# Optimization experiments

Hardware: AMD Instinct MI355X
Metric: run time of the kernel (lower is better)

## Reference

```python
import jax, jax.numpy as jnp
import numpy as np

EMBED_DIM = 1024
NUM_HEADS = 16
HEAD_DIM = EMBED_DIM // NUM_HEADS


def setup_inputs() -> dict:
    key = jax.random.key(0)
    ks = jax.random.split(key, 6)
    s = 1.0 / np.sqrt(EMBED_DIM)
    x = jax.random.normal(ks[0], (2, 2048, EMBED_DIM), dtype=jnp.float32)
    Wk = jax.random.uniform(ks[1], (EMBED_DIM, EMBED_DIM), jnp.float32, -s, s)
    Wq = jax.random.uniform(ks[2], (EMBED_DIM, EMBED_DIM), jnp.float32, -s, s)
    Wv = jax.random.uniform(ks[3], (EMBED_DIM, EMBED_DIM), jnp.float32, -s, s)
    Wo = jax.random.uniform(ks[4], (EMBED_DIM, EMBED_DIM), jnp.float32, -s, s)
    bo = jax.random.uniform(ks[5], (EMBED_DIM,), jnp.float32, -s, s)
    return {"x": x, "Wq": Wq, "Wk": Wk, "Wv": Wv, "Wo": Wo, "bo": bo}


def reference(x, Wq, Wk, Wv, Wo, bo):
    b, s, e = x.shape
    h, d = NUM_HEADS, HEAD_DIM
    scale = d ** (-0.5)
    # nn.Linear: y = x @ W.T ; here W stored as [out, in] -> use W.T
    q = (x @ Wq.T).reshape(b, s, h, d).transpose(0, 2, 1, 3)  # b h s d
    k = (x @ Wk.T).reshape(b, s, h, d).transpose(0, 2, 1, 3)
    v = (x @ Wv.T).reshape(b, s, h, d).transpose(0, 2, 1, 3)
    logits = jnp.einsum('bhqd,bhkd->bhqk', q, k) * scale
    attn = jax.nn.softmax(logits, axis=-1)
    out = jnp.einsum('bhqk,bhkd->bhqd', attn, v)
    out = out.transpose(0, 2, 1, 3).reshape(b, s, e)
    return out @ Wo.T + bo
```

## Files before the change

### kernel.cpp

```cpp
#include <hip/hip_runtime.h>
#include <hip/hip_bf16.h>

using short8 = __attribute__((ext_vector_type(8))) short;
using f32x4  = __attribute__((ext_vector_type(4))) float;
using uint4v = __attribute__((ext_vector_type(4))) unsigned;

#if __has_builtin(__builtin_amdgcn_exp2f)
#define EXP2(x) __builtin_amdgcn_exp2f(x)
#else
#define EXP2(x) exp2f(x)
#endif

#define SOFT_BARRIER()                                            \
    do {                                                          \
        asm volatile("s_waitcnt lgkmcnt(0)" ::: "memory");        \
        __builtin_amdgcn_s_barrier();                             \
    } while (0)

__device__ __forceinline__ short f2bf(float f) {
    union { float f; unsigned u; } v; v.f = f;
    unsigned r = v.u + 0x7fffu + ((v.u >> 16) & 1u);
    return (short)(r >> 16);
}
__device__ __forceinline__ unsigned pack_trunc(float a, float b) {
    union { float f; unsigned u; } ua, ub; ua.f = a; ub.f = b;
#if __has_builtin(__builtin_amdgcn_perm)
    return __builtin_amdgcn_perm(ub.u, ua.u, 0x07060302u);
#else
    return (ub.u & 0xFFFF0000u) | (ua.u >> 16);
#endif
}
__device__ __forceinline__ void async_copy16(const short* g, short* s) {
    __builtin_amdgcn_global_load_lds(
        (const __attribute__((address_space(1))) void*)g,
        (__attribute__((address_space(3))) void*)s, 16, 0, 0);
}

__global__ __launch_bounds__(256) void cvt_f32_bf16(
    const float* __restrict__ s0, const float* __restrict__ s1,
    const float* __restrict__ s2, const float* __restrict__ s3,
    const float* __restrict__ s4,
    short* __restrict__ d0, short* __restrict__ d1, short* __restrict__ d2,
    short* __restrict__ d3, short* __restrict__ d4) {
    const int bid = blockIdx.x;
    const float* s; short* d; int base;
    if (bid < 4096) {
        s = s0; d = d0; base = bid << 10;
    } else {
        const int r = bid - 4096;
        base = (r & 1023) << 10;
        switch (r >> 10) {
            case 0: s = s1; d = d1; break;
            case 1: s = s2; d = d2; break;
            case 2: s = s3; d = d3; break;
            default: s = s4; d = d4; break;
        }
    }
    const int idx = base + threadIdx.x * 4;
    float4 v = *(const float4*)(s + idx);
    short4 o;
    o.x = f2bf(v.x); o.y = f2bf(v.y); o.z = f2bf(v.z); o.w = f2bf(v.w);
    *(short4*)(d + idx) = o;
}

template <int MODE>
__device__ __forceinline__ void gemm_body(const short* __restrict__ A,
                                          const short* __restrict__ B,
                                          short* __restrict__ C,
                                          float scale,
                                          short* __restrict__ As,
                                          short* __restrict__ Bs) {
    constexpr int Kd = 1024, Nd = 1024, Sd = 2048;

    const int tid  = threadIdx.x;
    const int w    = tid >> 6, lane = tid & 63;
    const int quad = lane >> 4, l16 = lane & 15;
    const int xr   = l16 & 7;
    const int wm   = (w >> 1) * 64, wn = (w & 1) * 64;
    const int bm   = blockIdx.y * 128, bn = blockIdx.x * 128;

    f32x4 acc[4][4];
#pragma unroll
    for (int i = 0; i < 4; ++i)
#pragma unroll
        for (int j = 0; j < 4; ++j) acc[i][j] = (f32x4){0.f, 0.f, 0.f, 0.f};

    for (int k0 = 0; k0 < Kd; k0 += 64) {
        __syncthreads();
#pragma unroll
        for (int c = 0; c < 4; ++c) {
            int li   = c * 256 + tid;
            int row  = li >> 3;
            int gcol = ((li & 7) ^ (row & 7)) * 8;
            async_copy16(A + (size_t)(bm + row) * Kd + k0 + gcol, &As[li * 8]);
            async_copy16(B + (size_t)(bn + row) * Kd + k0 + gcol, &Bs[li * 8]);
        }
        __syncthreads();

#pragma unroll
        for (int kk = 0; kk < 2; ++kk) {
            short8 af[4], bfv[4];
#pragma unroll
            for (int mi = 0; mi < 4; ++mi) {
                const int r = wm + mi * 16 + l16;
                af[mi] = *(const short8*)(
                    &As[r * 64 + (((kk * 4 + quad) ^ xr) * 8)]);
            }
#pragma unroll
            for (int ni = 0; ni < 4; ++ni) {
                const int r = wn + ni * 16 + l16;
                bfv[ni] = *(const short8*)(
                    &Bs[r * 64 + (((kk * 4 + quad) ^ xr) * 8)]);
            }
#pragma unroll
            for (int mi = 0; mi < 4; ++mi)
#pragma unroll
                for (int ni = 0; ni < 4; ++ni) {
                    if constexpr (MODE == 2)
                        acc[mi][ni] = __builtin_amdgcn_mfma_f32_16x16x32_bf16(
                            bfv[ni], af[mi], acc[mi][ni], 0, 0, 0);
                    else
                        acc[mi][ni] = __builtin_amdgcn_mfma_f32_16x16x32_bf16(
                            af[mi], bfv[ni], acc[mi][ni], 0, 0, 0);
                }
        }
    }

    if constexpr (MODE == 2) {
#pragma unroll
        for (int mi = 0; mi < 4; ++mi) {
            const int m_g = bm + wm + mi * 16 + l16;
            const int b_  = m_g >> 11, s_ = m_g & 2047;
#pragma unroll
            for (int ni = 0; ni < 4; ++ni)
#pragma unroll
                for (int r = 0; r < 4; ++r) {
                    const int n_g = bn + wn + ni * 16 + quad * 4 + r;
                    C[(size_t)b_ * Nd * Sd + (size_t)n_g * Sd + s_] =
                        f2bf(acc[mi][ni][r]);
                }
        }
    } else {
#pragma unroll
        for (int ni = 0; ni < 4; ++ni) {
            const int colg = bn + wn + ni * 16 + l16;
#pragma unroll
            for (int mi = 0; mi < 4; ++mi)
#pragma unroll
                for (int r = 0; r < 4; ++r) {
                    const int rowg = bm + wm + mi * 16 + quad * 4 + r;
                    C[(size_t)rowg * Nd + colg] = f2bf(acc[mi][ni][r] * scale);
                }
        }
    }
}

#define CSC 0.18033688f

__global__ __launch_bounds__(256, 3) void proj_gemm(
    const short* __restrict__ X,
    const short* __restrict__ Wq, const short* __restrict__ Wk,
    const short* __restrict__ Wv,
    short* __restrict__ Qo, short* __restrict__ Ko, short* __restrict__ VTo) {
    __shared__ __align__(16) short As[128 * 64];
    __shared__ __align__(16) short Bs[128 * 64];
    if (blockIdx.z == 0)
        gemm_body<0>(X, Wq, Qo, CSC, As, Bs);
    else if (blockIdx.z == 1)
        gemm_body<0>(X, Wk, Ko, 1.0f, As, Bs);
    else
        gemm_body<2>(X, Wv, VTo, 1.0f, As, Bs);
}

__global__ __launch_bounds__(256, 2) void out_gemm(
    const short* __restrict__ A, const short* __restrict__ B,
    const float* __restrict__ bias, float* __restrict__ C) {
    constexpr int Kd = 1024, Nd = 1024;
    __shared__ __align__(16) short As[64 * 64];
    __shared__ __align__(16) short Bs[128 * 64];

    const int tid  = threadIdx.x;
    const int w    = tid >> 6, lane = tid & 63;
    const int quad = lane >> 4, l16 = lane & 15;
    const int xr   = l16 & 7;
    const int wm   = (w >> 1) * 32, wn = (w & 1) * 64;
    const int bm   = blockIdx.y * 64, bn = blockIdx.x * 128;

    f32x4 acc[2][4];
#pragma unroll
    for (int i = 0; i < 2; ++i)
#pragma unroll
        for (int j = 0; j < 4; ++j) acc[i][j] = (f32x4){0.f, 0.f, 0.f, 0.f};

    for (int k0 = 0; k0 < Kd; k0 += 64) {
        __syncthreads();
#pragma unroll
        for (int c = 0; c < 2; ++c) {
            int li   = c * 256 + tid;
            int row  = li >> 3;
            int gcol = ((li & 7) ^ (row & 7)) * 8;
            async_copy16(A + (size_t)(bm + row) * Kd + k0 + gcol, &As[li * 8]);
        }
#pragma unroll
        for (int c = 0; c < 4; ++c) {
            int li   = c * 256 + tid;
            int row  = li >> 3;
            int gcol = ((li & 7) ^ (row & 7)) * 8;
            async_copy16(B + (size_t)(bn + row) * Kd + k0 + gcol, &Bs[li * 8]);
        }
        __syncthreads();

#pragma unroll
        for (int kk = 0; kk < 2; ++kk) {
            short8 af[2], bfv[4];
#pragma unroll
            for (int mi = 0; mi < 2; ++mi) {
                const int r = wm + mi * 16 + l16;
                af[mi] = *(const short8*)(
                    &As[r * 64 + (((kk * 4 + quad) ^ xr) * 8)]);
            }
#pragma unroll
            for (int ni = 0; ni < 4; ++ni) {
                const int r = wn + ni * 16 + l16;
                bfv[ni] = *(const short8*)(
                    &Bs[r * 64 + (((kk * 4 + quad) ^ xr) * 8)]);
            }
#pragma unroll
            for (int mi = 0; mi < 2; ++mi)
#pragma unroll
                for (int ni = 0; ni < 4; ++ni)
                    acc[mi][ni] = __builtin_amdgcn_mfma_f32_16x16x32_bf16(
                        af[mi], bfv[ni], acc[mi][ni], 0, 0, 0);
        }
    }

#pragma unroll
    for (int ni = 0; ni < 4; ++ni) {
        const int colg = bn + wn + ni * 16 + l16;
        const float bv = bias[colg];
#pragma unroll
        for (int mi = 0; mi < 2; ++mi)
#pragma unroll
            for (int r = 0; r < 4; ++r) {
                const int rowg = bm + wm + mi * 16 + quad * 4 + r;
                C[(size_t)rowg * Nd + colg] = acc[mi][ni][r] + bv;
            }
    }
}

__global__ __launch_bounds__(256, 2) void attn_kernel(
    const short* __restrict__ Q, const short* __restrict__ K,
    const short* __restrict__ VT, short* __restrict__ O) {
    constexpr int S = 2048, E = 1024, NT = S / 64;
    __shared__ __align__(16) short Ks[2][64 * 64];
    __shared__ __align__(16) short Vs[3][64 * 64];

    const int tid  = threadIdx.x;
    const int w    = tid >> 6, lane = tid & 63;
    const int quad = lane >> 4, l16 = lane & 15;

    const int bid  = blockIdx.x;
    const int xcd  = bid & 7, slot = bid >> 3;
    const int qt   = slot & 15;
    const int bh   = xcd + ((slot >> 4) << 3);
    const int b    = bh >> 4, h = bh & 15;

    const int    q0   = qt * 128 + w * 32;
    const size_t base = (size_t)b * S * E;
    const size_t vtb  = (size_t)b * E * S;
    const int    hc   = h * 64;
    const int    xr   = l16 & 7;

    short8 aq[2][2];
#pragma unroll
    for (int qg = 0; qg < 2; ++qg) {
        const short* qp = Q + base + (size_t)(q0 + qg * 16 + l16) * E + hc + quad * 8;
        aq[qg][0] = *(const short8*)(qp);
        aq[qg][1] = *(const short8*)(qp + 32);
    }

    f32x4 oT[2][4], o_sum[2];
#pragma unroll
    for (int qg = 0; qg < 2; ++qg) {
        o_sum[qg] = (f32x4){0.f, 0.f, 0.f, 0.f};
#pragma unroll
        for (int i = 0; i < 4; ++i) oT[qg][i] = (f32x4){0.f, 0.f, 0.f, 0.f};
    }

    int          kdst[2], vdst0[2], vdst1[2];
    const short* kga[2];
    const short* vga[2];
#pragma unroll
    for (int c = 0; c < 2; ++c) {
        int li = c * 256 + tid, row = li >> 3, cc = li & 7;
        kdst[c] = row * 64 + ((cc ^ (row & 7)) * 8);
        int c0   = 4 * (cc >> 2) + 2 * (cc & 1);
        int boff = 4 * ((cc >> 1) & 1);
        vdst0[c] = row * 64 + ((c0 ^ (row & 7)) * 8) + boff;
        vdst1[c] = row * 64 + (((c0 + 1) ^ (row & 7)) * 8) + boff;
        kga[c]   = K + base + (size_t)row * E + hc + cc * 8;
        vga[c]   = VT + vtb + (size_t)(hc + row) * S + cc * 8;
    }

    short8 kr[2], vr[2];
    auto load_regs = [&](int t) {
#pragma unroll
        for (int c = 0; c < 2; ++c) {
            kr[c] = *(const short8*)(kga[c] + (size_t)t * 64 * E);
            vr[c] = *(const short8*)(vga[c] + t * 64);
        }
    };
    auto store_regs = [&](short* Kn, short* Vn) {
#pragma unroll
        for (int c = 0; c < 2; ++c) {
            *(short8*)(&Kn[kdst[c]]) = kr[c];
            short4 lo, hi;
            lo.x = vr[c][0]; lo.y = vr[c][1]; lo.z = vr[c][2]; lo.w = vr[c][3];
            hi.x = vr[c][4]; hi.y = vr[c][5]; hi.z = vr[c][6]; hi.w = vr[c][7];
            *(short4*)(&Vn[vdst0[c]]) = lo;
            *(short4*)(&Vn[vdst1[c]]) = hi;
        }
    };

    const short8 ones = (short8){0x3F80, 0x3F80, 0x3F80, 0x3F80,
                                 0x3F80, 0x3F80, 0x3F80, 0x3F80};
    const float  LB   = 0.00281502f;

    uint4v pkvA[2][2], pkvB[2][2];

    auto qk_half = [&](const short* Kc, uint4v (&pc)[2][2], int h) {
#pragma unroll
        for (int kh = 0; kh < 2; ++kh) {
            const int    kn  = h * 2 + kh;
            const short* kb  = &Kc[(kn * 16 + l16) * 64];
            short8       bk0 = *(const short8*)(kb + ((quad ^ xr) * 8));
            short8       bk1 = *(const short8*)(kb + (((quad + 4) ^ xr) * 8));
#pragma unroll
            for (int qg = 0; qg < 2; ++qg) {
                f32x4 a = (f32x4){LB, LB, LB, LB};
                a = __builtin_amdgcn_mfma_f32_16x16x32_bf16(bk0, aq[qg][0], a, 0, 0, 0);
                a = __builtin_amdgcn_mfma_f32_16x16x32_bf16(bk1, aq[qg][1], a, 0, 0, 0);
                pc[qg][h][kh * 2]     = pack_trunc(EXP2(a[0]), EXP2(a[1]));
                pc[qg][h][kh * 2 + 1] = pack_trunc(EXP2(a[2]), EXP2(a[3]));
            }
        }
    };
    auto pv_half = [&](const short* Vp, uint4v (&pp)[2][2], int ks) {
        short8 pf[2];
#pragma unroll
        for (int qg = 0; qg < 2; ++qg) {
            union { uint4v u; short8 s; } cv;
            cv.u   = pp[qg][ks];
            pf[qg] = cv.s;
            o_sum[qg] = __builtin_amdgcn_mfma_f32_16x16x32_bf16(
                ones, pf[qg], o_sum[qg], 0, 0, 0);
        }
#pragma unroll
        for (int ni = 0; ni < 4; ++ni) {
            const int rv = ni * 16 + l16;
            short8 vb =
                *(const short8*)(&Vp[rv * 64 + (((ks * 4 + quad) ^ xr) * 8)]);
#pragma unroll
            for (int qg = 0; qg < 2; ++qg)
                oT[qg][ni] = __builtin_amdgcn_mfma_f32_16x16x32_bf16(
                    vb, pf[qg], oT[qg][ni], 0, 0, 0);
        }
    };

    auto body = [&](int kt, uint4v (&pp)[2][2], uint4v (&pc)[2][2]) {
        if (kt + 1 < NT) {
            store_regs(Ks[(kt + 1) & 1], Vs[(kt + 1) % 3]);
            if (kt + 2 < NT) load_regs(kt + 2);
        }
        const short* Kc = Ks[kt & 1];
        const short* Vp = Vs[(kt - 1) % 3];
        __builtin_amdgcn_s_setprio(1);
        pv_half(Vp, pp, 0);
        qk_half(Kc, pc, 0);
        pv_half(Vp, pp, 1);
        qk_half(Kc, pc, 1);
        __builtin_amdgcn_s_setprio(0);
        SOFT_BARRIER();
    };

    load_regs(0);
    store_regs(Ks[0], Vs[0]);
    load_regs(1);
    SOFT_BARRIER();
    store_regs(Ks[1], Vs[1]);
    load_regs(2);
    __builtin_amdgcn_s_setprio(1);
    qk_half(Ks[0], pkvA, 0);
    qk_half(Ks[0], pkvA, 1);
    __builtin_amdgcn_s_setprio(0);
    SOFT_BARRIER();

#pragma unroll 1
    for (int kt = 1; kt < NT - 1; kt += 2) {
        body(kt, pkvA, pkvB);
        body(kt + 1, pkvB, pkvA);
    }
    body(NT - 1, pkvA, pkvB);
    __builtin_amdgcn_s_setprio(1);
    pv_half(Vs[(NT - 1) % 3], pkvB, 0);
    pv_half(Vs[(NT - 1) % 3], pkvB, 1);
    __builtin_amdgcn_s_setprio(0);

#pragma unroll
    for (int qg = 0; qg < 2; ++qg) {
        const float inv = 1.0f / o_sum[qg][0];
        const int   qg_ = q0 + qg * 16 + l16;
#pragma unroll
        for (int ni = 0; ni < 4; ++ni) {
            short4 ov;
            ov.x = f2bf(oT[qg][ni][0] * inv);
            ov.y = f2bf(oT[qg][ni][1] * inv);
            ov.z = f2bf(oT[qg][ni][2] * inv);
            ov.w = f2bf(oT[qg][ni][3] * inv);
            *(short4*)(&O[base + (size_t)qg_ * E + hc + ni * 16 + quad * 4]) = ov;
        }
    }
}

extern "C" void kernel_launch(void* const* d_in, const int* in_sizes, int n_in,
                              void* d_out, int out_size, void* d_ws, size_t ws_size,
                              hipStream_t stream) {
    const float* x  = (const float*)d_in[0];
    const float* Wq = (const float*)d_in[1];
    const float* Wk = (const float*)d_in[2];
    const float* Wv = (const float*)d_in[3];
    const float* Wo = (const float*)d_in[4];
    const float* bo = (const float*)d_in[5];
    float* out = (float*)d_out;

    constexpr int XN = 2 * 2048 * 1024;
    constexpr int WN = 1024 * 1024;

    short* Xb  = (short*)d_ws;
    short* Wqb = Xb + XN;
    short* Wkb = Wqb + WN;
    short* Wvb = Wkb + WN;
    short* Wob = Wvb + WN;
    short* Qb  = Wob + WN;
    short* Kb  = Qb + XN;
    short* VTb = Kb + XN;

    cvt_f32_bf16<<<dim3(8192), 256, 0, stream>>>(
        x, Wq, Wk, Wv, Wo, Xb, Wqb, Wkb, Wvb, Wob);
    proj_gemm<<<dim3(8, 32, 3), 256, 0, stream>>>(Xb, Wqb, Wkb, Wvb, Qb, Kb, VTb);
    attn_kernel<<<dim3(512), 256, 0, stream>>>(Qb, Kb, VTb, Xb );
    out_gemm<<<dim3(8, 64), 256, 0, stream>>>(Xb, Wob, bo, out);
}
```

Measured before the change: 168.5 us.

## Double-buffer GEMM LDS tiles with register-staged prefetch in projection and output kernels

Replaces the direct global-to-LDS async copies, which had two barriers per k-step, with a software pipeline. Each k-step loads the next tile into registers, stores it to the other of two LDS buffers, and computes on the current one, so only one barrier per step remains. Global load latency is meant to overlap with MFMA work. In exchange, LDS use doubles and register pressure rises, and proj_gemm's occupancy hint drops from 3 to 2 blocks per CU.

```diff
diff --git a/kernel.cpp b/kernel.cpp
--- a/kernel.cpp
+++ b/kernel.cpp
@@ -29,11 +29,6 @@
 #else
     return (ub.u & 0xFFFF0000u) | (ua.u >> 16);
 #endif
-}
-__device__ __forceinline__ void async_copy16(const short* g, short* s) {
-    __builtin_amdgcn_global_load_lds(
-        (const __attribute__((address_space(1))) void*)g,
-        (__attribute__((address_space(3))) void*)s, 16, 0, 0);
 }
 
 __global__ __launch_bounds__(256) void cvt_f32_bf16(
@@ -71,6 +66,7 @@
                                           short* __restrict__ As,
                                           short* __restrict__ Bs) {
     constexpr int Kd = 1024, Nd = 1024, Sd = 2048;
+    constexpr int BUF = 128 * 64;
 
     const int tid  = threadIdx.x;
     const int w    = tid >> 6, lane = tid & 63;
@@ -85,18 +81,34 @@
 #pragma unroll
         for (int j = 0; j < 4; ++j) acc[i][j] = (f32x4){0.f, 0.f, 0.f, 0.f};
 
-    for (int k0 = 0; k0 < Kd; k0 += 64) {
-        __syncthreads();
+    int sdst[4];
+    const short *aga[4], *bga[4];
+#pragma unroll
+    for (int c = 0; c < 4; ++c) {
+        const int li = c * 256 + tid, row = li >> 3;
+        const int gcol = ((li & 7) ^ (row & 7)) * 8;
+        sdst[c] = li * 8;
+        aga[c]  = A + (size_t)(bm + row) * Kd + gcol;
+        bga[c]  = B + (size_t)(bn + row) * Kd + gcol;
+    }
+
+    short8 ar[4], br[4];
+    auto load_st = [&](int k0) {
 #pragma unroll
         for (int c = 0; c < 4; ++c) {
-            int li   = c * 256 + tid;
-            int row  = li >> 3;
-            int gcol = ((li & 7) ^ (row & 7)) * 8;
-            async_copy16(A + (size_t)(bm + row) * Kd + k0 + gcol, &As[li * 8]);
-            async_copy16(B + (size_t)(bn + row) * Kd + k0 + gcol, &Bs[li * 8]);
-        }
-        __syncthreads();
-
+            ar[c] = *(const short8*)(aga[c] + k0);
+            br[c] = *(const short8*)(bga[c] + k0);
+        }
+    };
+    auto store_st = [&](short* Ad, short* Bd) {
+#pragma unroll
+        for (int c = 0; c < 4; ++c) {
+            *(short8*)(&Ad[sdst[c]]) = ar[c];
+            *(short8*)(&Bd[sdst[c]]) = br[c];
+        }
+    };
+
+    auto compute = [&](const short* Ac, const short* Bc) {
 #pragma unroll
         for (int kk = 0; kk < 2; ++kk) {
             short8 af[4], bfv[4];
@@ -104,13 +116,13 @@
             for (int mi = 0; mi < 4; ++mi) {
                 const int r = wm + mi * 16 + l16;
                 af[mi] = *(const short8*)(
-                    &As[r * 64 + (((kk * 4 + quad) ^ xr) * 8)]);
+                    &Ac[r * 64 + (((kk * 4 + quad) ^ xr) * 8)]);
             }
 #pragma unroll
             for (int ni = 0; ni < 4; ++ni) {
                 const int r = wn + ni * 16 + l16;
                 bfv[ni] = *(const short8*)(
-                    &Bs[r * 64 + (((kk * 4 + quad) ^ xr) * 8)]);
+                    &Bc[r * 64 + (((kk * 4 + quad) ^ xr) * 8)]);
             }
 #pragma unroll
             for (int mi = 0; mi < 4; ++mi)
@@ -124,6 +136,21 @@
                             af[mi], bfv[ni], acc[mi][ni], 0, 0, 0);
                 }
         }
+    };
+
+    load_st(0);
+    store_st(As, Bs);
+    load_st(64);
+    SOFT_BARRIER();
+
+#pragma unroll 1
+    for (int ks = 0; ks < 16; ++ks) {
+        if (ks + 1 < 16) {
+            store_st(As + ((ks + 1) & 1) * BUF, Bs + ((ks + 1) & 1) * BUF);
+            if (ks + 2 < 16) load_st((ks + 2) * 64);
+        }
+        compute(As + (ks & 1) * BUF, Bs + (ks & 1) * BUF);
+        SOFT_BARRIER();
     }
 
     if constexpr (MODE == 2) {
@@ -157,13 +184,13 @@
 
 #define CSC 0.18033688f
 
-__global__ __launch_bounds__(256, 3) void proj_gemm(
+__global__ __launch_bounds__(256, 2) void proj_gemm(
     const short* __restrict__ X,
     const short* __restrict__ Wq, const short* __restrict__ Wk,
     const short* __restrict__ Wv,
     short* __restrict__ Qo, short* __restrict__ Ko, short* __restrict__ VTo) {
-    __shared__ __align__(16) short As[128 * 64];
-    __shared__ __align__(16) short Bs[128 * 64];
+    __shared__ __align__(16) short As[2 * 128 * 64];
+    __shared__ __align__(16) short Bs[2 * 128 * 64];
     if (blockIdx.z == 0)
         gemm_body<0>(X, Wq, Qo, CSC, As, Bs);
     else if (blockIdx.z == 1)
@@ -176,8 +203,9 @@
     const short* __restrict__ A, const short* __restrict__ B,
     const float* __restrict__ bias, float* __restrict__ C) {
     constexpr int Kd = 1024, Nd = 1024;
-    __shared__ __align__(16) short As[64 * 64];
-    __shared__ __align__(16) short Bs[128 * 64];
+    constexpr int ABUF = 64 * 64, BBUF = 128 * 64;
+    __shared__ __align__(16) short As[2 * ABUF];
+    __shared__ __align__(16) short Bs[2 * BBUF];
 
     const int tid  = threadIdx.x;
     const int w    = tid >> 6, lane = tid & 63;
@@ -192,24 +220,38 @@
 #pragma unroll
         for (int j = 0; j < 4; ++j) acc[i][j] = (f32x4){0.f, 0.f, 0.f, 0.f};
 
-    for (int k0 = 0; k0 < Kd; k0 += 64) {
-        __syncthreads();
-#pragma unroll
-        for (int c = 0; c < 2; ++c) {
-            int li   = c * 256 + tid;
-            int row  = li >> 3;
-            int gcol = ((li & 7) ^ (row & 7)) * 8;
-            async_copy16(A + (size_t)(bm + row) * Kd + k0 + gcol, &As[li * 8]);
-        }
-#pragma unroll
-        for (int c = 0; c < 4; ++c) {
-            int li   = c * 256 + tid;
-            int row  = li >> 3;
-            int gcol = ((li & 7) ^ (row & 7)) * 8;
-            async_copy16(B + (size_t)(bn + row) * Kd + k0 + gcol, &Bs[li * 8]);
-        }
-        __syncthreads();
-
+    int asdst[2], bsdst[4];
+    const short *aga[2], *bga[4];
+#pragma unroll
+    for (int c = 0; c < 2; ++c) {
+        const int li = c * 256 + tid, row = li >> 3;
+        const int gcol = ((li & 7) ^ (row & 7)) * 8;
+        asdst[c] = li * 8;
+        aga[c]   = A + (size_t)(bm + row) * Kd + gcol;
+    }
+#pragma unroll
+    for (int c = 0; c < 4; ++c) {
+        const int li = c * 256 + tid, row = li >> 3;
+        const int gcol = ((li & 7) ^ (row & 7)) * 8;
+        bsdst[c] = li * 8;
+        bga[c]   = B + (size_t)(bn + row) * Kd + gcol;
+    }
+
+    short8 ar[2], br[4];
+    auto load_st = [&](int k0) {
+#pragma unroll
+        for (int c = 0; c < 2; ++c) ar[c] = *(const short8*)(aga[c] + k0);
+#pragma unroll
+        for (int c = 0; c < 4; ++c) br[c] = *(const short8*)(bga[c] + k0);
+    };
+    auto store_st = [&](short* Ad, short* Bd) {
+#pragma unroll
+        for (int c = 0; c < 2; ++c) *(short8*)(&Ad[asdst[c]]) = ar[c];
+#pragma unroll
+        for (int c = 0; c < 4; ++c) *(short8*)(&Bd[bsdst[c]]) = br[c];
+    };
+
+    auto compute = [&](const short* Ac, const short* Bc) {
 #pragma unroll
         for (int kk = 0; kk < 2; ++kk) {
             short8 af[2], bfv[4];
@@ -217,13 +259,13 @@
             for (int mi = 0; mi < 2; ++mi) {
                 const int r = wm + mi * 16 + l16;
                 af[mi] = *(const short8*)(
-                    &As[r * 64 + (((kk * 4 + quad) ^ xr) * 8)]);
+                    &Ac[r * 64 + (((kk * 4 + quad) ^ xr) * 8)]);
             }
 #pragma unroll
             for (int ni = 0; ni < 4; ++ni) {
                 const int r = wn + ni * 16 + l16;
                 bfv[ni] = *(const short8*)(
-                    &Bs[r * 64 + (((kk * 4 + quad) ^ xr) * 8)]);
+                    &Bc[r * 64 + (((kk * 4 + quad) ^ xr) * 8)]);
             }
 #pragma unroll
             for (int mi = 0; mi < 2; ++mi)
@@ -232,6 +274,21 @@
                     acc[mi][ni] = __builtin_amdgcn_mfma_f32_16x16x32_bf16(
                         af[mi], bfv[ni], acc[mi][ni], 0, 0, 0);
         }
+    };
+
+    load_st(0);
+    store_st(As, Bs);
+    load_st(64);
+    SOFT_BARRIER();
+
+#pragma unroll 1
+    for (int ks = 0; ks < 16; ++ks) {
+        if (ks + 1 < 16) {
+            store_st(As + ((ks + 1) & 1) * ABUF, Bs + ((ks + 1) & 1) * BBUF);
+            if (ks + 2 < 16) load_st((ks + 2) * 64);
+        }
+        compute(As + (ks & 1) * ABUF, Bs + (ks & 1) * BBUF);
+        SOFT_BARRIER();
     }
 
 #pragma unroll
```

Result: slower. 186.0 us (+10.4%).
